# Kernel optimization log

Measured on AMD Instinct MI355X. Metric: run time of the kernel, lower is better.

Reference implementation:

```python
import jax, jax.numpy as jnp
import numpy as np

NEG_SLOPE = 0.2  # PyG GATConv default

def gat_layer(x, src, dst, W, a_src, a_dst, b, N):
    # h = W x  (PyG applies linear before attention)
    h = x @ W                                   # [N, hid]
    al_src = h @ a_src                          # [N]
    al_dst = h @ a_dst                          # [N]
    e = jax.nn.leaky_relu(al_src[src] + al_dst[dst], NEG_SLOPE)  # [E]
    # segment softmax over incoming edges of each destination node
    m = jax.ops.segment_max(e, dst, num_segments=N)
    e = jnp.exp(e - m[dst])
    s = jax.ops.segment_sum(e, dst, num_segments=N)
    coef = e / s[dst]                           # [E]
    out = jax.ops.segment_sum(h[src] * coef[:, None], dst, num_segments=N)
    return out + b

def setup_inputs() -> dict:
    key = jax.random.key(0)
    ks = jax.random.split(key, 12)
    N, E, in_dim, hid, out_dim, G = 100000, 1600000, 128, 64, 1, 256
    x = jax.random.normal(ks[0], (N, in_dim), dtype=jnp.float32)
    edge_index = jax.random.randint(ks[1], (2, E), 0, N, dtype=jnp.int64)
    batch = jnp.sort(jax.random.randint(ks[2], (N,), 0, G, dtype=jnp.int64))
    def glorot(k, shape):
        lim = float(np.sqrt(6.0 / (shape[0] + shape[-1])))
        return jax.random.uniform(k, shape, jnp.float32, -lim, lim)
    return {
        "x": x, "edge_index": edge_index, "batch": batch,
        "W1": glorot(ks[3], (in_dim, hid)),
        "a_src1": glorot(ks[4], (hid,)), "a_dst1": glorot(ks[5], (hid,)),
        "b1": jnp.zeros((hid,), jnp.float32),
        "W2": glorot(ks[6], (hid, hid)),
        "a_src2": glorot(ks[7], (hid,)), "a_dst2": glorot(ks[8], (hid,)),
        "b2": jnp.zeros((hid,), jnp.float32),
        "Wfc": glorot(ks[9], (hid, out_dim)),
        "bfc": jnp.zeros((out_dim,), jnp.float32),
    }

def reference(x, edge_index, batch, W1, a_src1, a_dst1, b1, W2, a_src2, a_dst2, b2, Wfc, bfc):
    N = x.shape[0]
    G = 256  # number of graphs in the batch
    # add self-loops (PyG GATConv default add_self_loops=True)
    loops = jnp.arange(N, dtype=edge_index.dtype)
    src = jnp.concatenate([edge_index[0], loops])
    dst = jnp.concatenate([edge_index[1], loops])
    h = jax.nn.elu(gat_layer(x, src, dst, W1, a_src1, a_dst1, b1, N))
    h = jax.nn.elu(gat_layer(h, src, dst, W2, a_src2, a_dst2, b2, N))
    # global mean pool over graph ids
    sums = jax.ops.segment_sum(h, batch, num_segments=G)
    cnts = jax.ops.segment_sum(jnp.ones((N,), h.dtype), batch, num_segments=G)
    pooled = sums / jnp.maximum(cnts, 1.0)[:, None]
    return pooled @ Wfc + bfc
```

## Files before the change

### kernel.cpp

```cpp
#include <hip/hip_runtime.h>
#include <hip/hip_bf16.h>
#include <cstdint>


#define BIN_SHIFT 8
#define BIN_NODES 256
#define BIN_CAP 6144
#define PLACE_CHUNK 2048

typedef __attribute__((ext_vector_type(8))) short bf16x8;
typedef __attribute__((ext_vector_type(4))) float f32x4;

__device__ __forceinline__ float wave_reduce_sum(float v) {
#pragma unroll
  for (int off = 32; off > 0; off >>= 1) v += __shfl_xor(v, off, 64);
  return v;
}

__device__ __forceinline__ unsigned short f2bf(float f) {
  unsigned int u = __float_as_uint(f);
  u += 0x7fffu + ((u >> 16) & 1u);
  return (unsigned short)(u >> 16);
}
__device__ __forceinline__ float bf2f(unsigned short u) {
  return __uint_as_float(((unsigned int)u) << 16);
}


__global__ __launch_bounds__(256) void setup_kernel(
    const float* __restrict__ W1, unsigned short* __restrict__ w1thi,
    unsigned short* __restrict__ w1tlo, const float* __restrict__ W2,
    unsigned short* __restrict__ w2thi, unsigned short* __restrict__ w2tlo,
    const int* __restrict__ batch, int* __restrict__ gstart,
    int* __restrict__ binCursor, float* __restrict__ pool, int N, int G, int NB) {
  const int b = blockIdx.x;
  const int t = threadIdx.x;
  if (b < 32) {
    int idx = b * 256 + t;
    int n = idx & 63, k = idx >> 6;
    float v = W1[(size_t)k * 64 + n];
    unsigned short h = f2bf(v);
    w1thi[(size_t)n * 128 + k] = h;
    w1tlo[(size_t)n * 128 + k] = f2bf(v - bf2f(h));
  } else if (b < 48) {
    int idx = (b - 32) * 256 + t;
    int n = idx & 63, k = idx >> 6;
    float v = W2[(size_t)k * 64 + n];
    unsigned short h = f2bf(v);
    w2thi[(size_t)n * 64 + k] = h;
    w2tlo[(size_t)n * 64 + k] = f2bf(v - bf2f(h));
  } else if (b < 50) {
    int g = (b - 48) * 256 + t;
    if (g <= G) {
      int lo = 0, hi = N;
      while (lo < hi) {
        int mid = (lo + hi) >> 1;
        if (batch[mid] < g) lo = mid + 1;
        else hi = mid;
      }
      gstart[g] = lo;
    }
  } else if (b < 52) {
    int i = (b - 50) * 256 + t;
    if (i < NB) binCursor[i] = 0;
  } else {
    int i = (b - 52) * 256 + t;
    pool[i] = 0.f;
  }
}


__global__ __launch_bounds__(256) void bin_place_kernel(
    const int* __restrict__ ei, int E, int M, int NB,
    int* __restrict__ binCursor, unsigned int* __restrict__ binned) {
  __shared__ int cur[512];
  __shared__ int res[512];
  const int t = threadIdx.x;
  const int cbase = blockIdx.x * PLACE_CHUNK;

  for (int i = t; i < NB; i += 256) cur[i] = 0;
  __syncthreads();

  unsigned int pk[PLACE_CHUNK / 256];
  int br[PLACE_CHUNK / 256];
#pragma unroll
  for (int j = 0; j < PLACE_CHUNK / 256; ++j) {
    int i = cbase + t + j * 256;
    if (i < M) {
      int s, d;
      if (i < E) { s = ei[i]; d = ei[E + i]; } else { s = d = i - E; }
      int b = d >> BIN_SHIFT;
      int r = atomicAdd(&cur[b], 1);
      pk[j] = ((unsigned int)(d & (BIN_NODES - 1)) << 24) | (unsigned int)s;
      br[j] = (b << 16) | r;
    } else {
      br[j] = -1;
    }
  }
  __syncthreads();
  for (int i = t; i < NB; i += 256) {
    int c = cur[i];
    res[i] = c ? atomicAdd(&binCursor[i], c) : 0;
  }
  __syncthreads();
#pragma unroll
  for (int j = 0; j < PLACE_CHUNK / 256; ++j) {
    if (br[j] >= 0) {
      int b = br[j] >> 16;
      int pos = res[b] + (br[j] & 0xFFFF);
      if (pos < BIN_CAP) binned[(size_t)b * BIN_CAP + pos] = pk[j];
    }
  }
}

__global__ __launch_bounds__(512) void csr_finalize_kernel(
    const unsigned int* __restrict__ binned, const int* __restrict__ binCursor,
    int* __restrict__ rowbeg, int* __restrict__ rowend, int* __restrict__ csrc,
    int N, int NB) {
  __shared__ int cnt[256];
  __shared__ int off[256];
  __shared__ int wsum[8];
  const int b = blockIdx.x;
  const int t = threadIdx.x;
  const int nodeBase = b << BIN_SHIFT;
  const int eBase = b * BIN_CAP;
  const int cntE = binCursor[b];

  if (t < 256) cnt[t] = 0;
  __syncthreads();
  for (int i = t; i < cntE; i += 512) {
    atomicAdd(&cnt[binned[eBase + i] >> 24], 1);
  }
  __syncthreads();
  const int lane = t & 63, wv = t >> 6;
  int v = (t < 256) ? cnt[t] : 0;
  int x = v;
#pragma unroll
  for (int o = 1; o < 64; o <<= 1) {
    int u = __shfl_up(x, o, 64);
    if (lane >= o) x += u;
  }
  if (t < 256 && lane == 63) wsum[wv] = x;
  __syncthreads();
  if (t < 256) {
    int woff = 0;
    for (int j = 0; j < wv; j++) woff += wsum[j];
    const int o = woff + x - v;
    off[t] = o;
    int node = nodeBase + t;
    if (node < N) {
      rowbeg[node] = eBase + o;
      rowend[node] = eBase + o + v;
    }
    cnt[t] = o;
  }
  __syncthreads();
  for (int i = t; i < cntE; i += 512) {
    unsigned int pk = binned[eBase + i];
    int r = atomicAdd(&cnt[pk >> 24], 1);
    csrc[eBase + r] = (int)(pk & 0xFFFFFFu);
  }
}


template <int KDIM>
__global__ __launch_bounds__(256) void gemm_mfma(
    const float* __restrict__ A, const unsigned short* __restrict__ Wt_hi,
    const unsigned short* __restrict__ Wt_lo, unsigned short* __restrict__ hb,
    const float* __restrict__ a_src, const float* __restrict__ a_dst,
    float* __restrict__ alsrc, float* __restrict__ aldst, int N) {
  __shared__ unsigned short Ah[64][40], Al[64][40], Bh[64][40], Bl[64][40];
  const int block_m = blockIdx.x * 64;
  const int t = threadIdx.x;
  const int lane = t & 63;
  const int m0 = (t >> 6) * 16;
  const int lc = lane & 15;
  const int lr = lane >> 4;
  const int srow = t >> 2;
  const int skslot = (t & 3) * 8;

  f32x4 acc[4] = {};

  for (int kc = 0; kc < KDIM; kc += 32) {
    {
      int gn = block_m + srow;
      if (gn >= N) gn = N - 1;
      const float4 v0 = *(const float4*)(A + (size_t)gn * KDIM + kc + skslot);
      const float4 v1 = *(const float4*)(A + (size_t)gn * KDIM + kc + skslot + 4);
      float v[8] = {v0.x, v0.y, v0.z, v0.w, v1.x, v1.y, v1.z, v1.w};
      unsigned short h8[8], l8[8];
#pragma unroll
      for (int j = 0; j < 8; ++j) {
        h8[j] = f2bf(v[j]);
        l8[j] = f2bf(v[j] - bf2f(h8[j]));
      }
      *(uint4*)&Ah[srow][skslot] = *(const uint4*)h8;
      *(uint4*)&Al[srow][skslot] = *(const uint4*)l8;
    }
    {
      const uint4 wh = *(const uint4*)(Wt_hi + (size_t)srow * KDIM + kc + skslot);
      const uint4 wl = *(const uint4*)(Wt_lo + (size_t)srow * KDIM + kc + skslot);
      *(uint4*)&Bh[srow][skslot] = wh;
      *(uint4*)&Bl[srow][skslot] = wl;
    }
    __syncthreads();

    const bf16x8 ah = *(const bf16x8*)&Ah[m0 + lc][lr * 8];
    const bf16x8 al = *(const bf16x8*)&Al[m0 + lc][lr * 8];
#pragma unroll
    for (int nf = 0; nf < 4; ++nf) {
      const bf16x8 bh = *(const bf16x8*)&Bh[nf * 16 + lc][lr * 8];
      const bf16x8 bl = *(const bf16x8*)&Bl[nf * 16 + lc][lr * 8];
      acc[nf] = __builtin_amdgcn_mfma_f32_16x16x32_bf16(ah, bh, acc[nf], 0, 0, 0);
      acc[nf] = __builtin_amdgcn_mfma_f32_16x16x32_bf16(ah, bl, acc[nf], 0, 0, 0);
      acc[nf] = __builtin_amdgcn_mfma_f32_16x16x32_bf16(al, bh, acc[nf], 0, 0, 0);
    }
    __syncthreads();
  }

  float as4[4], ad4[4];
#pragma unroll
  for (int nf = 0; nf < 4; ++nf) {
    as4[nf] = a_src[nf * 16 + lc];
    ad4[nf] = a_dst[nf * 16 + lc];
  }
#pragma unroll
  for (int r = 0; r < 4; ++r) {
    const int gn = block_m + m0 + lr * 4 + r;
    float ps = 0.f, pd = 0.f;
#pragma unroll
    for (int nf = 0; nf < 4; ++nf) {
      const float v = acc[nf][r];
      if (gn < N) hb[(size_t)gn * 64 + nf * 16 + lc] = f2bf(v);
      ps += v * as4[nf];
      pd += v * ad4[nf];
    }
#pragma unroll
    for (int off = 1; off < 16; off <<= 1) {
      ps += __shfl_xor(ps, off, 64);
      pd += __shfl_xor(pd, off, 64);
    }
    if (lc == 0 && gn < N) {
      alsrc[gn] = ps;
      aldst[gn] = pd;
    }
  }
}

template <int ELU>
__global__ __launch_bounds__(256) void spmm_fused_kernel(
    const int* __restrict__ rowbeg, const int* __restrict__ rowend,
    const int* __restrict__ csrc,
    const float* __restrict__ alsrc, const float* __restrict__ aldst,
    const unsigned short* __restrict__ hb, const float* __restrict__ bias,
    float* __restrict__ outbuf, int N) {
  const int t = threadIdx.x;
  const int l = t & 15;
  const int gb = t & 48;
  const int half = l >> 3;
  const int f0 = (l & 7) * 8;
  const int node = blockIdx.x * 16 + (t >> 4);
  if (node >= N) return;
  const int start = rowbeg[node];
  const int end = rowend[node];
  const float ad = aldst[node];

  float ssum = 0.f;
  float acc[8] = {};

  int i0 = start + l;
  bool v0 = i0 < end;
  int s = v0 ? csrc[i0] : 0;
  float w;
  {
    float e = alsrc[s] + ad;
    e = (e > 0.f) ? e : 0.2f * e;
    w = v0 ? __expf(fminf(e, 80.f)) : 0.f;
  }

  for (int base = start; base < end; base += 16) {
    int in = base + 16 + l;
    bool vn = in < end;
    int sn = vn ? csrc[in] : 0;
    float aln = alsrc[sn];

    uint4 u[8];
#pragma unroll
    for (int j = 0; j < 8; ++j) {
      int sj = __shfl(s, gb + 2 * j + half, 64);
      u[j] = *(const uint4*)(hb + (size_t)sj * 64 + f0);
    }

    ssum += w;
#pragma unroll
    for (int j = 0; j < 8; ++j) {
      float wj = __shfl(w, gb + 2 * j + half, 64);
      acc[0] += wj * __uint_as_float(u[j].x << 16);
      acc[1] += wj * __uint_as_float(u[j].x & 0xFFFF0000u);
      acc[2] += wj * __uint_as_float(u[j].y << 16);
      acc[3] += wj * __uint_as_float(u[j].y & 0xFFFF0000u);
      acc[4] += wj * __uint_as_float(u[j].z << 16);
      acc[5] += wj * __uint_as_float(u[j].z & 0xFFFF0000u);
      acc[6] += wj * __uint_as_float(u[j].w << 16);
      acc[7] += wj * __uint_as_float(u[j].w & 0xFFFF0000u);
    }

    float en = aln + ad;
    en = (en > 0.f) ? en : 0.2f * en;
    w = vn ? __expf(fminf(en, 80.f)) : 0.f;
    s = sn;
  }

#pragma unroll
  for (int k = 0; k < 8; ++k) acc[k] += __shfl_xor(acc[k], 8, 64);
#pragma unroll
  for (int off = 1; off < 16; off <<= 1) ssum += __shfl_xor(ssum, off, 64);

  if (half == 0) {
    float inv = 1.0f / ssum;
    float r[8];
#pragma unroll
    for (int k = 0; k < 8; ++k) r[k] = acc[k] * inv;
    if (ELU) {
      const float4 b40 = *(const float4*)(bias + f0);
      const float4 b41 = *(const float4*)(bias + f0 + 4);
      r[0] += b40.x; r[1] += b40.y; r[2] += b40.z; r[3] += b40.w;
      r[4] += b41.x; r[5] += b41.y; r[6] += b41.z; r[7] += b41.w;
#pragma unroll
      for (int k = 0; k < 8; ++k) r[k] = (r[k] > 0.f) ? r[k] : expm1f(r[k]);
    }
    *(float4*)(outbuf + (size_t)node * 64 + f0) = make_float4(r[0], r[1], r[2], r[3]);
    *(float4*)(outbuf + (size_t)node * 64 + f0 + 4) = make_float4(r[4], r[5], r[6], r[7]);
  }
}

__global__ __launch_bounds__(256) void post_pool_kernel(
    const float* __restrict__ acc, const float* __restrict__ bias,
    const int* __restrict__ batch, float* __restrict__ pool, int N) {
  __shared__ float4 red4[16][17];
  __shared__ int sB[16];
  __shared__ int uni;
  const int t = threadIdx.x;
  const int ln = t >> 4;
  const int f4 = t & 15;
  const int base = blockIdx.x * 16;
  const int node = base + ln;

  if (t < 16) {
    int nn = base + t;
    sB[t] = (nn < N) ? batch[nn] : -1;
  }
  __syncthreads();
  if (t == 0) {
    int u = (base + 15 < N);
    for (int i = 1; i < 16; i++) u &= (sB[i] == sB[0]);
    uni = u;
  }

  float4 v = make_float4(0.f, 0.f, 0.f, 0.f);
  if (node < N) {
    v = *(const float4*)(acc + ((size_t)node * 16 + f4) * 4);
    const float4 b4 = *(const float4*)(bias + f4 * 4);
    v.x += b4.x; v.y += b4.y; v.z += b4.z; v.w += b4.w;
    v.x = (v.x > 0.f) ? v.x : expm1f(v.x);
    v.y = (v.y > 0.f) ? v.y : expm1f(v.y);
    v.z = (v.z > 0.f) ? v.z : expm1f(v.z);
    v.w = (v.w > 0.f) ? v.w : expm1f(v.w);
  }
  red4[ln][f4] = v;
  __syncthreads();

  if (t < 64) {
    const float* rf = (const float*)red4;
    if (uni) {
      float s = 0.f;
#pragma unroll
      for (int n = 0; n < 16; n++) s += rf[n * 68 + t];
      atomicAdd(&pool[(size_t)sB[0] * 64 + t], s);
    } else {
      for (int n = 0; n < 16; n++) {
        int g = sB[n];
        if (g >= 0) atomicAdd(&pool[(size_t)g * 64 + t], rf[n * 68 + t]);
      }
    }
  }
}

__global__ void final_kernel(const float* __restrict__ pool, const int* __restrict__ gstart,
                             const float* __restrict__ Wfc, const float* __restrict__ bfc,
                             float* __restrict__ out, int G) {
  int wid = (blockIdx.x * blockDim.x + threadIdx.x) >> 6;
  int lane = threadIdx.x & 63;
  if (wid >= G) return;
  float c = (float)max(gstart[wid + 1] - gstart[wid], 1);
  float v = pool[(size_t)wid * 64 + lane] * (1.0f / c) * Wfc[lane];
  v = wave_reduce_sum(v);
  if (lane == 0) out[wid] = v + bfc[0];
}


extern "C" void kernel_launch(void* const* d_in, const int* in_sizes, int n_in,
                              void* d_out, int out_size, void* d_ws, size_t ws_size,
                              hipStream_t stream) {
  const float* x     = (const float*)d_in[0];
  const int*   ei    = (const int*)d_in[1];
  const int*   batch = (const int*)d_in[2];
  const float* W1    = (const float*)d_in[3];
  const float* asrc1 = (const float*)d_in[4];
  const float* adst1 = (const float*)d_in[5];
  const float* b1    = (const float*)d_in[6];
  const float* W2    = (const float*)d_in[7];
  const float* asrc2 = (const float*)d_in[8];
  const float* adst2 = (const float*)d_in[9];
  const float* b2    = (const float*)d_in[10];
  const float* Wfc   = (const float*)d_in[11];
  const float* bfc   = (const float*)d_in[12];
  float* out = (float*)d_out;

  const int N = in_sizes[0] / 128;
  const int E = in_sizes[1] / 2;
  const int G = 256;
  const int M = E + N;
  const int NB = (N + BIN_NODES - 1) >> BIN_SHIFT;

  char* p = (char*)d_ws;
  auto alloc = [&](size_t bytes) {
    char* r = p;
    p += (bytes + 255) & ~size_t(255);
    return r;
  };
  float*          h1e    = (float*)alloc((size_t)N * 64 * 4);
  float*          accbuf = (float*)alloc((size_t)N * 64 * 4);
  unsigned short* hb     = (unsigned short*)alloc((size_t)N * 64 * 2);
  float* alsrc  = (float*)alloc((size_t)N * 4);
  float* aldst  = (float*)alloc((size_t)N * 4);
  int*   rowbeg = (int*)alloc((size_t)N * 4);
  int*   rowend = (int*)alloc((size_t)N * 4);
  int*   csrc   = (int*)alloc((size_t)NB * BIN_CAP * 4);
  unsigned int* binned = (unsigned int*)alloc((size_t)NB * BIN_CAP * 4);
  int*   binCursor = (int*)alloc((size_t)NB * 4);
  float* pool   = (float*)alloc((size_t)G * 64 * 4);
  int*   gstart = (int*)alloc((size_t)(G + 1) * 4);
  unsigned short* w1thi = (unsigned short*)alloc((size_t)64 * 128 * 2);
  unsigned short* w1tlo = (unsigned short*)alloc((size_t)64 * 128 * 2);
  unsigned short* w2thi = (unsigned short*)alloc((size_t)64 * 64 * 2);
  unsigned short* w2tlo = (unsigned short*)alloc((size_t)64 * 64 * 2);

  setup_kernel<<<116, 256, 0, stream>>>(W1, w1thi, w1tlo, W2, w2thi, w2tlo,
                                        batch, gstart, binCursor, pool, N, G, NB);
  bin_place_kernel<<<(M + PLACE_CHUNK - 1) / PLACE_CHUNK, 256, 0, stream>>>(
      ei, E, M, NB, binCursor, binned);
  csr_finalize_kernel<<<NB, 512, 0, stream>>>(binned, binCursor, rowbeg, rowend,
                                              csrc, N, NB);

  gemm_mfma<128><<<(N + 63) / 64, 256, 0, stream>>>(x, w1thi, w1tlo, hb, asrc1, adst1,
                                                    alsrc, aldst, N);
  spmm_fused_kernel<1><<<(N + 15) / 16, 256, 0, stream>>>(rowbeg, rowend, csrc, alsrc,
                                                          aldst, hb, b1, h1e, N);

  gemm_mfma<64><<<(N + 63) / 64, 256, 0, stream>>>(h1e, w2thi, w2tlo, hb, asrc2, adst2,
                                                   alsrc, aldst, N);
  spmm_fused_kernel<0><<<(N + 15) / 16, 256, 0, stream>>>(rowbeg, rowend, csrc, alsrc,
                                                          aldst, hb, nullptr, accbuf, N);
  post_pool_kernel<<<(N + 15) / 16, 256, 0, stream>>>(accbuf, b2, batch, pool, N);

  final_kernel<<<(G * 64 + 255) / 256, 256, 0, stream>>>(pool, gstart, Wfc, bfc, out, G);
}
```

Baseline: 268.4 us.

## Fuse layer-2 bias/ELU and mean-pool into SpMM; shrink CSR bins to 128 nodes

Layer-2 SpMM now applies bias and ELU itself and atomically adds its per-node results into the pooled sums. It pre-reduces across the four nodes in a wave when they share a graph id. This removes the separate post_pool kernel and the N×64 fp32 accumulation buffer round-trip. Separately, CSR bins shrink from 256 to 128 nodes with a smaller capacity, doubling the bin count and the finalize block count for more parallelism. Costs are more global atomics per wave, higher risk of bin overflow with the smaller cap, and larger shared arrays in bin_place.

```diff
diff --git a/kernel.cpp b/kernel.cpp
--- a/kernel.cpp
+++ b/kernel.cpp
@@ -3,9 +3,9 @@
 #include <cstdint>
 
 
-#define BIN_SHIFT 8
-#define BIN_NODES 256
-#define BIN_CAP 6144
+#define BIN_SHIFT 7
+#define BIN_NODES 128
+#define BIN_CAP 3584
 #define PLACE_CHUNK 2048
 
 typedef __attribute__((ext_vector_type(8))) short bf16x8;
@@ -60,11 +60,11 @@
       }
       gstart[g] = lo;
     }
-  } else if (b < 52) {
+  } else if (b < 54) {
     int i = (b - 50) * 256 + t;
     if (i < NB) binCursor[i] = 0;
   } else {
-    int i = (b - 52) * 256 + t;
+    int i = (b - 54) * 256 + t;
     pool[i] = 0.f;
   }
 }
@@ -73,8 +73,8 @@
 __global__ __launch_bounds__(256) void bin_place_kernel(
     const int* __restrict__ ei, int E, int M, int NB,
     int* __restrict__ binCursor, unsigned int* __restrict__ binned) {
-  __shared__ int cur[512];
-  __shared__ int res[512];
+  __shared__ int cur[1024];
+  __shared__ int res[1024];
   const int t = threadIdx.x;
   const int cbase = blockIdx.x * PLACE_CHUNK;
 
@@ -117,36 +117,32 @@
     const unsigned int* __restrict__ binned, const int* __restrict__ binCursor,
     int* __restrict__ rowbeg, int* __restrict__ rowend, int* __restrict__ csrc,
     int N, int NB) {
-  __shared__ int cnt[256];
-  __shared__ int off[256];
-  __shared__ int wsum[8];
+  __shared__ int cnt[128];
+  __shared__ int wsum[2];
   const int b = blockIdx.x;
   const int t = threadIdx.x;
   const int nodeBase = b << BIN_SHIFT;
   const int eBase = b * BIN_CAP;
   const int cntE = binCursor[b];
 
-  if (t < 256) cnt[t] = 0;
+  if (t < 128) cnt[t] = 0;
   __syncthreads();
   for (int i = t; i < cntE; i += 512) {
     atomicAdd(&cnt[binned[eBase + i] >> 24], 1);
   }
   __syncthreads();
   const int lane = t & 63, wv = t >> 6;
-  int v = (t < 256) ? cnt[t] : 0;
+  int v = (t < 128) ? cnt[t] : 0;
   int x = v;
 #pragma unroll
   for (int o = 1; o < 64; o <<= 1) {
     int u = __shfl_up(x, o, 64);
     if (lane >= o) x += u;
   }
-  if (t < 256 && lane == 63) wsum[wv] = x;
-  __syncthreads();
-  if (t < 256) {
-    int woff = 0;
-    for (int j = 0; j < wv; j++) woff += wsum[j];
-    const int o = woff + x - v;
-    off[t] = o;
+  if (t < 128 && lane == 63) wsum[wv] = x;
+  __syncthreads();
+  if (t < 128) {
+    const int o = ((wv == 1) ? wsum[0] : 0) + x - v;
     int node = nodeBase + t;
     if (node < N) {
       rowbeg[node] = eBase + o;
@@ -247,13 +243,14 @@
   }
 }
 
-template <int ELU>
+template <int MODE>
 __global__ __launch_bounds__(256) void spmm_fused_kernel(
     const int* __restrict__ rowbeg, const int* __restrict__ rowend,
     const int* __restrict__ csrc,
     const float* __restrict__ alsrc, const float* __restrict__ aldst,
     const unsigned short* __restrict__ hb, const float* __restrict__ bias,
-    float* __restrict__ outbuf, int N) {
+    float* __restrict__ outbuf, const int* __restrict__ batch,
+    float* __restrict__ pool, int N) {
   const int t = threadIdx.x;
   const int l = t & 15;
   const int gb = t & 48;
@@ -316,71 +313,44 @@
 #pragma unroll
   for (int off = 1; off < 16; off <<= 1) ssum += __shfl_xor(ssum, off, 64);
 
-  if (half == 0) {
-    float inv = 1.0f / ssum;
-    float r[8];
-#pragma unroll
-    for (int k = 0; k < 8; ++k) r[k] = acc[k] * inv;
-    if (ELU) {
-      const float4 b40 = *(const float4*)(bias + f0);
-      const float4 b41 = *(const float4*)(bias + f0 + 4);
-      r[0] += b40.x; r[1] += b40.y; r[2] += b40.z; r[3] += b40.w;
-      r[4] += b41.x; r[5] += b41.y; r[6] += b41.z; r[7] += b41.w;
-#pragma unroll
-      for (int k = 0; k < 8; ++k) r[k] = (r[k] > 0.f) ? r[k] : expm1f(r[k]);
-    }
-    *(float4*)(outbuf + (size_t)node * 64 + f0) = make_float4(r[0], r[1], r[2], r[3]);
-    *(float4*)(outbuf + (size_t)node * 64 + f0 + 4) = make_float4(r[4], r[5], r[6], r[7]);
-  }
-}
-
-__global__ __launch_bounds__(256) void post_pool_kernel(
-    const float* __restrict__ acc, const float* __restrict__ bias,
-    const int* __restrict__ batch, float* __restrict__ pool, int N) {
-  __shared__ float4 red4[16][17];
-  __shared__ int sB[16];
-  __shared__ int uni;
-  const int t = threadIdx.x;
-  const int ln = t >> 4;
-  const int f4 = t & 15;
-  const int base = blockIdx.x * 16;
-  const int node = base + ln;
-
-  if (t < 16) {
-    int nn = base + t;
-    sB[t] = (nn < N) ? batch[nn] : -1;
-  }
-  __syncthreads();
-  if (t == 0) {
-    int u = (base + 15 < N);
-    for (int i = 1; i < 16; i++) u &= (sB[i] == sB[0]);
-    uni = u;
-  }
-
-  float4 v = make_float4(0.f, 0.f, 0.f, 0.f);
-  if (node < N) {
-    v = *(const float4*)(acc + ((size_t)node * 16 + f4) * 4);
-    const float4 b4 = *(const float4*)(bias + f4 * 4);
-    v.x += b4.x; v.y += b4.y; v.z += b4.z; v.w += b4.w;
-    v.x = (v.x > 0.f) ? v.x : expm1f(v.x);
-    v.y = (v.y > 0.f) ? v.y : expm1f(v.y);
-    v.z = (v.z > 0.f) ? v.z : expm1f(v.z);
-    v.w = (v.w > 0.f) ? v.w : expm1f(v.w);
-  }
-  red4[ln][f4] = v;
-  __syncthreads();
-
-  if (t < 64) {
-    const float* rf = (const float*)red4;
+  const float inv = 1.0f / ssum;
+  float r[8];
+#pragma unroll
+  for (int k = 0; k < 8; ++k) r[k] = acc[k] * inv;
+  {
+    const float4 b40 = *(const float4*)(bias + f0);
+    const float4 b41 = *(const float4*)(bias + f0 + 4);
+    r[0] += b40.x; r[1] += b40.y; r[2] += b40.z; r[3] += b40.w;
+    r[4] += b41.x; r[5] += b41.y; r[6] += b41.z; r[7] += b41.w;
+#pragma unroll
+    for (int k = 0; k < 8; ++k) r[k] = (r[k] > 0.f) ? r[k] : expm1f(r[k]);
+  }
+
+  if (MODE == 1) {
+    if (half == 0) {
+      *(float4*)(outbuf + (size_t)node * 64 + f0) = make_float4(r[0], r[1], r[2], r[3]);
+      *(float4*)(outbuf + (size_t)node * 64 + f0 + 4) = make_float4(r[4], r[5], r[6], r[7]);
+    }
+  } else {
+    const int g = batch[node];
+    const bool uni = __all(g == __shfl_xor(g, 16, 64)) &&
+                     __all(g == __shfl_xor(g, 32, 64));
     if (uni) {
-      float s = 0.f;
-#pragma unroll
-      for (int n = 0; n < 16; n++) s += rf[n * 68 + t];
-      atomicAdd(&pool[(size_t)sB[0] * 64 + t], s);
+#pragma unroll
+      for (int k = 0; k < 8; ++k) {
+        r[k] += __shfl_xor(r[k], 16, 64);
+        r[k] += __shfl_xor(r[k], 32, 64);
+      }
+      if ((t & 63) < 8) {
+#pragma unroll
+        for (int k = 0; k < 8; ++k)
+          atomicAdd(&pool[(size_t)g * 64 + f0 + k], r[k]);
+      }
     } else {
-      for (int n = 0; n < 16; n++) {
-        int g = sB[n];
-        if (g >= 0) atomicAdd(&pool[(size_t)g * 64 + t], rf[n * 68 + t]);
+      if (half == 0) {
+#pragma unroll
+        for (int k = 0; k < 8; ++k)
+          atomicAdd(&pool[(size_t)g * 64 + f0 + k], r[k]);
       }
     }
   }
@@ -430,7 +400,6 @@
     return r;
   };
   float*          h1e    = (float*)alloc((size_t)N * 64 * 4);
-  float*          accbuf = (float*)alloc((size_t)N * 64 * 4);
   unsigned short* hb     = (unsigned short*)alloc((size_t)N * 64 * 2);
   float* alsrc  = (float*)alloc((size_t)N * 4);
   float* aldst  = (float*)alloc((size_t)N * 4);
@@ -446,7 +415,7 @@
   unsigned short* w2thi = (unsigned short*)alloc((size_t)64 * 64 * 2);
   unsigned short* w2tlo = (unsigned short*)alloc((size_t)64 * 64 * 2);
 
-  setup_kernel<<<116, 256, 0, stream>>>(W1, w1thi, w1tlo, W2, w2thi, w2tlo,
+  setup_kernel<<<118, 256, 0, stream>>>(W1, w1thi, w1tlo, W2, w2thi, w2tlo,
                                         batch, gstart, binCursor, pool, N, G, NB);
   bin_place_kernel<<<(M + PLACE_CHUNK - 1) / PLACE_CHUNK, 256, 0, stream>>>(
       ei, E, M, NB, binCursor, binned);
@@ -455,14 +424,13 @@
 
   gemm_mfma<128><<<(N + 63) / 64, 256, 0, stream>>>(x, w1thi, w1tlo, hb, asrc1, adst1,
                                                     alsrc, aldst, N);
-  spmm_fused_kernel<1><<<(N + 15) / 16, 256, 0, stream>>>(rowbeg, rowend, csrc, alsrc,
-                                                          aldst, hb, b1, h1e, N);
+  spmm_fused_kernel<1><<<(N + 15) / 16, 256, 0, stream>>>(
+      rowbeg, rowend, csrc, alsrc, aldst, hb, b1, h1e, nullptr, nullptr, N);
 
   gemm_mfma<64><<<(N + 63) / 64, 256, 0, stream>>>(h1e, w2thi, w2tlo, hb, asrc2, adst2,
                                                    alsrc, aldst, N);
-  spmm_fused_kernel<0><<<(N + 15) / 16, 256, 0, stream>>>(rowbeg, rowend, csrc, alsrc,
-                                                          aldst, hb, nullptr, accbuf, N);
-  post_pool_kernel<<<(N + 15) / 16, 256, 0, stream>>>(accbuf, b2, batch, pool, N);
+  spmm_fused_kernel<0><<<(N + 15) / 16, 256, 0, stream>>>(
+      rowbeg, rowend, csrc, alsrc, aldst, hb, b2, nullptr, batch, pool, N);
 
   final_kernel<<<(G * 64 + 255) / 256, 256, 0, stream>>>(pool, gstart, Wfc, bfc, out, G);
 }
```

Result: slower. 393.5 us (+46.6%).
